# Performance work log

Hardware: AMD Instinct MI355X
Metric: run time of the kernel (lower is better)

Reference implementation:

```python
import jax, jax.numpy as jnp
import numpy as np

V, E, HD, K = 100000, 128, 256, 9
B, T = 128, 512
H = HD // 2  # per-direction hidden size


def setup_inputs() -> dict:
    key = jax.random.key(0)
    ks = jax.random.split(key, 16)
    s = 0.1
    rn = lambda k, shape: jax.random.normal(k, shape, jnp.float32) * s
    sentences = jax.random.randint(ks[0], (B, T), 0, V, dtype=jnp.int32)
    lengths = jax.random.randint(ks[1], (B,), 1, T + 1, dtype=jnp.int32)
    return {
        'sentences': sentences,
        'lengths': lengths,
        'embed': rn(ks[2], (V, E)),
        'Wih_f': rn(ks[3], (4 * H, E)), 'Whh_f': rn(ks[4], (4 * H, H)),
        'bih_f': rn(ks[5], (4 * H,)), 'bhh_f': rn(ks[6], (4 * H,)),
        'Wih_b': rn(ks[7], (4 * H, E)), 'Whh_b': rn(ks[8], (4 * H, H)),
        'bih_b': rn(ks[9], (4 * H,)), 'bhh_b': rn(ks[10], (4 * H,)),
        'W_out': rn(ks[11], (K, HD)), 'b_out': rn(ks[12], (K,)),
        'start_t': rn(ks[13], (K,)), 'end_t': rn(ks[14], (K,)),
        'trans': rn(ks[15], (K, K)),
    }


def _lstm(x, mask, Wih, Whh, bih, bhh, reverse):
    # x: [B,T,E], mask: [B,T] bool. Replicates packed-sequence semantics:
    # state frozen and output zeroed at padding positions (padding is trailing,
    # so reverse=True starts fresh at each sequence's true end).
    Bv, Hv = x.shape[0], Whh.shape[1]
    bias = bih + bhh

    def step(carry, inp):
        h, c = carry
        x_t, m_t = inp  # [B,E], [B,1]
        gates = x_t @ Wih.T + h @ Whh.T + bias  # [B,4H]
        i, f, g, o = jnp.split(gates, 4, axis=-1)  # torch gate order i,f,g,o
        c_new = jax.nn.sigmoid(f) * c + jax.nn.sigmoid(i) * jnp.tanh(g)
        h_new = jax.nn.sigmoid(o) * jnp.tanh(c_new)
        h = jnp.where(m_t, h_new, h)
        c = jnp.where(m_t, c_new, c)
        return (h, c), h * m_t.astype(h.dtype)

    init = (jnp.zeros((Bv, Hv), x.dtype), jnp.zeros((Bv, Hv), x.dtype))
    xs = (jnp.swapaxes(x, 0, 1), jnp.swapaxes(mask, 0, 1)[..., None])
    _, hs = jax.lax.scan(step, init, xs, reverse=reverse)
    return jnp.swapaxes(hs, 0, 1)  # [B,T,H]


def _emissions(sentences, mask, embed, Wih_f, Whh_f, bih_f, bhh_f,
               Wih_b, Whh_b, bih_b, bhh_b, W_out, b_out):
    x = embed[sentences]  # [B,T,E] (dropout is identity at inference)
    hf = _lstm(x, mask, Wih_f, Whh_f, bih_f, bhh_f, reverse=False)
    hb = _lstm(x, mask, Wih_b, Whh_b, bih_b, bhh_b, reverse=True)
    h = jnp.concatenate([hf, hb], axis=-1)  # [B,T,2H]
    return jnp.einsum('btd,kd->btk', h, W_out) + b_out  # [B,T,K]


def _viterbi(em, mask, start_t, end_t, trans):
    # torchcrf-style batched Viterbi decode. em: [B,T,K], mask: [B,T] bool.
    Kv = em.shape[-1]
    ident = jnp.arange(Kv, dtype=jnp.int32)[None]  # identity backpointers for pads
    score0 = start_t[None] + em[:, 0]  # [B,K]

    def step(score, inp):
        em_t, m_t = inp  # [B,K], [B,1]
        cand = score[:, :, None] + trans[None] + em_t[:, None, :]  # [B,K_prev,K_cur]
        new_score = cand.max(axis=1)
        idx = cand.argmax(axis=1).astype(jnp.int32)  # [B,K]
        score = jnp.where(m_t, new_score, score)
        idx = jnp.where(m_t, idx, ident)
        return score, idx

    xs = (jnp.swapaxes(em[:, 1:], 0, 1), jnp.swapaxes(mask[:, 1:], 0, 1)[..., None])
    score, hist = jax.lax.scan(step, score0, xs)  # hist: [T-1,B,K]
    score = score + end_t[None]
    last_tag = jnp.argmax(score, axis=-1).astype(jnp.int32)  # [B]

    def back(tag, idx_t):
        prev = jnp.take_along_axis(idx_t, tag[:, None], axis=1)[:, 0]
        return prev, prev

    _, tags_prev = jax.lax.scan(back, last_tag, hist, reverse=True)  # [T-1,B]
    tags = jnp.swapaxes(jnp.concatenate([tags_prev, last_tag[None]], axis=0), 0, 1)
    return jnp.where(mask, tags, 0), score.max(axis=-1)


def reference(sentences, lengths, embed, Wih_f, Whh_f, bih_f, bhh_f,
              Wih_b, Whh_b, bih_b, bhh_b, W_out, b_out, start_t, end_t, trans):
    mask = jnp.arange(sentences.shape[1])[None] < lengths[:, None]  # [B,T]
    em = _emissions(sentences, mask, embed, Wih_f, Whh_f, bih_f, bhh_f,
                    Wih_b, Whh_b, bih_b, bhh_b, W_out, b_out)
    tags, _ = _viterbi(em, mask, start_t, end_t, trans)
    return tags  # [B,T] int32, padded positions set to 0
```

## Files before the change

### kernel.cpp

```cpp
#include <hip/hip_runtime.h>
#include <cmath>

#define B_  128
#define T_  512
#define E_  128
#define H_  128
#define G4  512
#define K_  9

__global__ __launch_bounds__(256, 2)
void proj_gemm(const int* __restrict__ sent, const float* __restrict__ embed,
               const float* __restrict__ Wf, const float* __restrict__ Wb,
               const float* __restrict__ bif, const float* __restrict__ bhf,
               const float* __restrict__ bib, const float* __restrict__ bhb,
               float* __restrict__ proj, int t0f, int Tc)
{
  __shared__ __align__(16) float Al[128 * 64];
  __shared__ __align__(16) float Bl[128 * 64];
  const int tid   = threadIdx.x;
  const int ntile = blockIdx.x;
  const int mtile = blockIdx.y;
  const int tpb   = Tc >> 6;
  const int b     = mtile / tpb;
  const int toff  = (mtile - b * tpb) << 6;
  const int dir   = ntile >> 3;
  const int t0    = dir ? (T_ - t0f - Tc) : t0f;
  const float* __restrict__ W = dir ? Wb : Wf;
  const int n0 = (ntile & 7) << 6;

  {
    const int r  = tid & 63;
    const int kc = tid >> 6;
    const int t  = t0 + toff + r;
    const int vid = sent[b * T_ + t];
    const float* arow = embed + (size_t)vid * E_ + kc * 32;
    const float* brow = W + (size_t)(n0 + r) * E_ + kc * 32;
#pragma unroll
    for (int q = 0; q < 8; ++q) {
      float4 av = *(const float4*)(arow + q * 4);
      float4 bv = *(const float4*)(brow + q * 4);
      int k0 = kc * 32 + q * 4;
      Al[(k0 + 0) * 64 + r] = av.x; Al[(k0 + 1) * 64 + r] = av.y;
      Al[(k0 + 2) * 64 + r] = av.z; Al[(k0 + 3) * 64 + r] = av.w;
      Bl[(k0 + 0) * 64 + r] = bv.x; Bl[(k0 + 1) * 64 + r] = bv.y;
      Bl[(k0 + 2) * 64 + r] = bv.z; Bl[(k0 + 3) * 64 + r] = bv.w;
    }
  }
  __syncthreads();

  const int mg = tid & 15, ng = tid >> 4;
  float acc[4][4] = {};
#pragma unroll 8
  for (int k = 0; k < 128; ++k) {
    float4 a  = *(const float4*)&Al[k * 64 + mg * 4];
    float4 bb = *(const float4*)&Bl[k * 64 + ng * 4];
    acc[0][0] += a.x * bb.x; acc[0][1] += a.x * bb.y; acc[0][2] += a.x * bb.z; acc[0][3] += a.x * bb.w;
    acc[1][0] += a.y * bb.x; acc[1][1] += a.y * bb.y; acc[1][2] += a.y * bb.z; acc[1][3] += a.y * bb.w;
    acc[2][0] += a.z * bb.x; acc[2][1] += a.z * bb.y; acc[2][2] += a.z * bb.z; acc[2][3] += a.z * bb.w;
    acc[3][0] += a.w * bb.x; acc[3][1] += a.w * bb.y; acc[3][2] += a.w * bb.z; acc[3][3] += a.w * bb.w;
  }

  const float* bi = dir ? bib : bif;
  const float* bh = dir ? bhb : bhf;
  const int nl = ng * 4;
  float4 bias;
  bias.x = bi[n0 + nl + 0] + bh[n0 + nl + 0];
  bias.y = bi[n0 + nl + 1] + bh[n0 + nl + 1];
  bias.z = bi[n0 + nl + 2] + bh[n0 + nl + 2];
  bias.w = bi[n0 + nl + 3] + bh[n0 + nl + 3];
#pragma unroll
  for (int i = 0; i < 4; ++i) {
    const int tloc = toff + mg * 4 + i;
    float4 o;
    o.x = acc[i][0] + bias.x; o.y = acc[i][1] + bias.y;
    o.z = acc[i][2] + bias.z; o.w = acc[i][3] + bias.w;
    *(float4*)&proj[((size_t)(b * Tc + tloc)) * 1024 + dir * G4 + n0 + nl] = o;
  }
}

__global__ __launch_bounds__(512, 2)
void lstm_chunk(const float* __restrict__ proj,
                const float* __restrict__ Whf, const float* __restrict__ Whb,
                const int* __restrict__ lengths,
                float* __restrict__ hs,
                float* __restrict__ sh, float* __restrict__ sc,
                int t0f, int Tc, int first)
{
  const int dir = blockIdx.x;
  const int b   = blockIdx.y;
  const int tid = threadIdx.x;
  const float* __restrict__ Whh = dir ? Whb : Whf;
  __shared__ __align__(16) float h_lds[H_];
  __shared__ float gates[G4];

  float w[128];
  {
    const float* wr = Whh + (size_t)tid * H_;
#pragma unroll
    for (int k = 0; k < 128; k += 4) {
      float4 v = *(const float4*)(wr + k);
      w[k] = v.x; w[k + 1] = v.y; w[k + 2] = v.z; w[k + 3] = v.w;
    }
  }
#pragma unroll
  for (int k = 0; k < 128; ++k) asm volatile("" : "+v"(w[k]));

  const int len = lengths[b];
  const int t0  = dir ? (T_ - t0f - Tc) : t0f;
  float c = 0.f;
  if (tid < H_) {
    if (first) {
      h_lds[tid] = 0.f;
    } else {
      h_lds[tid] = sh[(dir * B_ + b) * H_ + tid];
      c          = sc[(dir * B_ + b) * H_ + tid];
    }
  }
  __syncthreads();

  const float* projp = proj + (size_t)b * Tc * 1024 + dir * G4 + tid;
  float pv = projp[(size_t)(dir ? (Tc - 1) : 0) * 1024];
  for (int s = 0; s < Tc; ++s) {
    const int tc = dir ? (Tc - 1 - s) : s;
    const int t  = t0 + tc;
    float nv = 0.f;
    if (s + 1 < Tc) {
      const int tcn = dir ? (Tc - 2 - s) : (s + 1);
      nv = projp[(size_t)tcn * 1024];
    }
    float a0 = 0.f, a1 = 0.f, a2 = 0.f, a3 = 0.f;
#pragma unroll
    for (int k4 = 0; k4 < 32; ++k4) {
      float4 h4 = *(const float4*)&h_lds[k4 * 4];
      a0 += w[4 * k4 + 0] * h4.x; a1 += w[4 * k4 + 1] * h4.y;
      a2 += w[4 * k4 + 2] * h4.z; a3 += w[4 * k4 + 3] * h4.w;
    }
    float acc = pv + (a0 + a1) + (a2 + a3);
    const int blk = tid >> 7;
    gates[tid] = (blk == 2) ? tanhf(acc) : 1.f / (1.f + expf(-acc));
    __syncthreads();
    if (tid < H_) {
      float gi = gates[tid], gf = gates[tid + 128];
      float gg = gates[tid + 256], go = gates[tid + 384];
      float cn = gf * c + gi * gg;
      float hn = go * tanhf(cn);
      bool  m  = (t < len);
      float hold = h_lds[tid];
      c = m ? cn : c;
      h_lds[tid] = m ? hn : hold;
      hs[(size_t)(b * T_ + t) * 256 + dir * H_ + tid] = m ? hn : 0.f;
    }
    __syncthreads();
    pv = nv;
  }
  if (tid < H_) {
    sh[(dir * B_ + b) * H_ + tid] = h_lds[tid];
    sc[(dir * B_ + b) * H_ + tid] = c;
  }
}

__global__ __launch_bounds__(256)
void emis_kernel(const float* __restrict__ hs, const float* __restrict__ Wout,
                 const float* __restrict__ bout, float* __restrict__ em)
{
  __shared__ __align__(16) float Wl[K_ * 256];
  const int tid = threadIdx.x;
  for (int i = tid; i < K_ * 256; i += 256) Wl[i] = Wout[i];
  __syncthreads();
  const int m = blockIdx.x * 256 + tid;
  const float* h = hs + (size_t)m * 256;
  float acc[K_] = {};
#pragma unroll 4
  for (int kk = 0; kk < 64; ++kk) {
    float4 h4 = *(const float4*)(h + kk * 4);
#pragma unroll
    for (int k9 = 0; k9 < K_; ++k9) {
      float4 w4 = *(const float4*)&Wl[k9 * 256 + kk * 4];
      acc[k9] += h4.x * w4.x + h4.y * w4.y + h4.z * w4.z + h4.w * w4.w;
    }
  }
#pragma unroll
  for (int k9 = 0; k9 < K_; ++k9) em[(size_t)m * K_ + k9] = acc[k9] + bout[k9];
}

__global__ __launch_bounds__(64)
void viterbi_kernel(const float* __restrict__ em, const int* __restrict__ lengths,
                    const float* __restrict__ st, const float* __restrict__ en,
                    const float* __restrict__ trans, int* __restrict__ tags)
{
  const int b    = blockIdx.x;
  const int lane = threadIdx.x;
  __shared__ unsigned char hist[(T_ - 1) * 16];
  const int len = lengths[b];
  float tr[K_];
#pragma unroll
  for (int j = 0; j < K_; ++j) tr[j] = (lane < K_) ? trans[j * K_ + lane] : 0.f;
  float s = (lane < K_) ? st[lane] + em[(size_t)(b * T_) * K_ + lane] : -1e30f;
  for (int t = 1; t < len; ++t) {
    float best = -1e30f; int bj = 0;
#pragma unroll
    for (int j = 0; j < K_; ++j) {
      float v = __shfl(s, j) + tr[j];
      if (v > best) { best = v; bj = j; }
    }
    if (lane < K_) {
      s = best + em[(size_t)(b * T_ + t) * K_ + lane];
      hist[(t - 1) * 16 + lane] = (unsigned char)bj;
    }
  }
  float fs = (lane < K_) ? s + en[lane] : -1e30f;
  float best = -1e30f; int last = 0;
#pragma unroll
  for (int j = 0; j < K_; ++j) {
    float v = __shfl(fs, j);
    if (v > best) { best = v; last = j; }
  }
  __syncthreads();
  if (lane == 0) {
    int tag = last;
    tags[b * T_ + len - 1] = tag;
    for (int t = len - 2; t >= 0; --t) {
      tag = hist[t * 16 + tag];
      tags[b * T_ + t] = tag;
    }
  }
  for (int t = len + lane; t < T_; t += 64) tags[b * T_ + t] = 0;
}

extern "C" void kernel_launch(void* const* d_in, const int* in_sizes, int n_in,
                              void* d_out, int out_size, void* d_ws, size_t ws_size,
                              hipStream_t stream)
{
  const int*   sent  = (const int*)d_in[0];
  const int*   lens  = (const int*)d_in[1];
  const float* embed = (const float*)d_in[2];
  const float* Wif   = (const float*)d_in[3];
  const float* Whf   = (const float*)d_in[4];
  const float* bif   = (const float*)d_in[5];
  const float* bhf   = (const float*)d_in[6];
  const float* Wib   = (const float*)d_in[7];
  const float* Whb   = (const float*)d_in[8];
  const float* bib   = (const float*)d_in[9];
  const float* bhb   = (const float*)d_in[10];
  const float* Wout  = (const float*)d_in[11];
  const float* bout  = (const float*)d_in[12];
  const float* stt   = (const float*)d_in[13];
  const float* ent   = (const float*)d_in[14];
  const float* trans = (const float*)d_in[15];
  int* tags = (int*)d_out;

  float* ws   = (float*)d_ws;
  float* hs   = ws;
  float* em   = hs + (size_t)B_ * T_ * 256;
  float* sh   = em + (size_t)B_ * T_ * K_;
  float* sc   = sh + (size_t)2 * B_ * H_;
  float* proj = sc + (size_t)2 * B_ * H_;
  const size_t fixed_bytes = (size_t)(proj - ws) * sizeof(float);

  int Tc = 512;
  while (Tc > 64 && fixed_bytes + (size_t)B_ * Tc * 1024 * sizeof(float) > ws_size)
    Tc >>= 1;

  const int nch = T_ / Tc;
  for (int c2 = 0; c2 < nch; ++c2) {
    const int t0f = c2 * Tc;
    dim3 g1(16, B_ * (Tc >> 6));
    hipLaunchKernelGGL(proj_gemm, g1, dim3(256), 0, stream,
                       sent, embed, Wif, Wib, bif, bhf, bib, bhb, proj, t0f, Tc);
    dim3 g2(2, B_);
    hipLaunchKernelGGL(lstm_chunk, g2, dim3(512), 0, stream,
                       proj, Whf, Whb, lens, hs, sh, sc, t0f, Tc, (int)(c2 == 0));
  }
  hipLaunchKernelGGL(emis_kernel, dim3((B_ * T_) / 256), dim3(256), 0, stream,
                     hs, Wout, bout, em);
  hipLaunchKernelGGL(viterbi_kernel, dim3(B_), dim3(64), 0, stream,
                     em, lens, stt, ent, trans, tags);
}
```

Measured before the change: 976.4 us.

## Compute LSTM gates in-wave via shuffles with double-buffered hidden state

Recurrent LSTM step is remapped so each lane handles two gate rows over half of the hidden dimension, combining K-halves and gate groups with cross-lane shuffles instead of a shared gates array. All four gates for a hidden unit now land in the same wave, so the cell update is done redundantly per lane and the hidden vector is double-buffered in LDS. This removes one of the two block barriers per timestep along with the LDS gate round trip. The cost is extra shuffles and redundant elementwise work, and the row-to-lane mapping must be exactly right.

New measurement: 940.7 us. 3.6% less time.

```diff
diff --git a/kernel.cpp b/kernel.cpp
--- a/kernel.cpp
+++ b/kernel.cpp
@@ -89,73 +89,94 @@
   const int dir = blockIdx.x;
   const int b   = blockIdx.y;
   const int tid = threadIdx.x;
+  const int l   = tid & 63;
+  const int wv  = tid >> 6;
+  const int u   = wv * 16 + (l & 15);
+  const int gp  = (l >> 4) & 1;
+  const int kh  = l >> 5;
+  const int rowA = u + (gp ? 256 : 0);
+  const int rowB = rowA + 128;
   const float* __restrict__ Whh = dir ? Whb : Whf;
-  __shared__ __align__(16) float h_lds[H_];
-  __shared__ float gates[G4];
-
-  float w[128];
+  __shared__ __align__(16) float h_hist[2][H_];
+
+  float wA[64], wB[64];
   {
-    const float* wr = Whh + (size_t)tid * H_;
-#pragma unroll
-    for (int k = 0; k < 128; k += 4) {
-      float4 v = *(const float4*)(wr + k);
-      w[k] = v.x; w[k + 1] = v.y; w[k + 2] = v.z; w[k + 3] = v.w;
-    }
-  }
-#pragma unroll
-  for (int k = 0; k < 128; ++k) asm volatile("" : "+v"(w[k]));
+    const float* wra = Whh + (size_t)rowA * H_ + kh * 64;
+    const float* wrb = Whh + (size_t)rowB * H_ + kh * 64;
+#pragma unroll
+    for (int k = 0; k < 64; k += 4) {
+      float4 va = *(const float4*)(wra + k);
+      float4 vb = *(const float4*)(wrb + k);
+      wA[k] = va.x; wA[k + 1] = va.y; wA[k + 2] = va.z; wA[k + 3] = va.w;
+      wB[k] = vb.x; wB[k + 1] = vb.y; wB[k + 2] = vb.z; wB[k + 3] = vb.w;
+    }
+  }
+#pragma unroll
+  for (int k = 0; k < 64; ++k) {
+    asm volatile("" : "+v"(wA[k]));
+    asm volatile("" : "+v"(wB[k]));
+  }
 
   const int len = lengths[b];
   const int t0  = dir ? (T_ - t0f - Tc) : t0f;
-  float c = 0.f;
-  if (tid < H_) {
-    if (first) {
-      h_lds[tid] = 0.f;
-    } else {
-      h_lds[tid] = sh[(dir * B_ + b) * H_ + tid];
-      c          = sc[(dir * B_ + b) * H_ + tid];
-    }
-  }
-  __syncthreads();
-
-  const float* projp = proj + (size_t)b * Tc * 1024 + dir * G4 + tid;
-  float pv = projp[(size_t)(dir ? (Tc - 1) : 0) * 1024];
+  float c = 0.f, h_reg = 0.f;
+  if (!first) {
+    c     = sc[(dir * B_ + b) * H_ + u];
+    h_reg = sh[(dir * B_ + b) * H_ + u];
+  }
+  if (l < 16) h_hist[1][u] = h_reg;
+  __syncthreads();
+
+  const float* projpA = proj + (size_t)b * Tc * 1024 + dir * G4 + rowA;
+  const float* projpB = projpA + 128;
+  const int tc00 = dir ? (Tc - 1) : 0;
+  float pvA = projpA[(size_t)tc00 * 1024];
+  float pvB = projpB[(size_t)tc00 * 1024];
+
   for (int s = 0; s < Tc; ++s) {
     const int tc = dir ? (Tc - 1 - s) : s;
     const int t  = t0 + tc;
-    float nv = 0.f;
+    float nvA = 0.f, nvB = 0.f;
     if (s + 1 < Tc) {
       const int tcn = dir ? (Tc - 2 - s) : (s + 1);
-      nv = projp[(size_t)tcn * 1024];
-    }
+      nvA = projpA[(size_t)tcn * 1024];
+      nvB = projpB[(size_t)tcn * 1024];
+    }
+    const float* hp = h_hist[(s + 1) & 1] + kh * 64;
     float a0 = 0.f, a1 = 0.f, a2 = 0.f, a3 = 0.f;
 #pragma unroll
-    for (int k4 = 0; k4 < 32; ++k4) {
-      float4 h4 = *(const float4*)&h_lds[k4 * 4];
-      a0 += w[4 * k4 + 0] * h4.x; a1 += w[4 * k4 + 1] * h4.y;
-      a2 += w[4 * k4 + 2] * h4.z; a3 += w[4 * k4 + 3] * h4.w;
-    }
-    float acc = pv + (a0 + a1) + (a2 + a3);
-    const int blk = tid >> 7;
-    gates[tid] = (blk == 2) ? tanhf(acc) : 1.f / (1.f + expf(-acc));
+    for (int k4 = 0; k4 < 16; ++k4) {
+      float4 h4 = *(const float4*)&hp[k4 * 4];
+      a0 += wA[4 * k4 + 0] * h4.x; a1 += wA[4 * k4 + 1] * h4.y;
+      a0 += wA[4 * k4 + 2] * h4.z; a1 += wA[4 * k4 + 3] * h4.w;
+      a2 += wB[4 * k4 + 0] * h4.x; a3 += wB[4 * k4 + 1] * h4.y;
+      a2 += wB[4 * k4 + 2] * h4.z; a3 += wB[4 * k4 + 3] * h4.w;
+    }
+    float sA = a0 + a1; sA += __shfl_xor(sA, 32); sA += pvA;
+    float sB = a2 + a3; sB += __shfl_xor(sB, 32); sB += pvB;
+    const float gA = gp ? tanhf(sA) : 1.f / (1.f + expf(-sA));
+    const float gB = 1.f / (1.f + expf(-sB));
+    const float xA = __shfl_xor(gA, 16);
+    const float xB = __shfl_xor(gB, 16);
+    const float gi = gp ? xA : gA;
+    const float gf = gp ? xB : gB;
+    const float gg = gp ? gA : xA;
+    const float go = gp ? gB : xB;
+    const float cn = gf * c + gi * gg;
+    const float hn = go * tanhf(cn);
+    const bool  m  = (t < len);
+    c     = m ? cn : c;
+    h_reg = m ? hn : h_reg;
+    if (l < 16) {
+      h_hist[s & 1][u] = h_reg;
+      hs[(size_t)(b * T_ + t) * 256 + dir * H_ + u] = m ? hn : 0.f;
+    }
     __syncthreads();
-    if (tid < H_) {
-      float gi = gates[tid], gf = gates[tid + 128];
-      float gg = gates[tid + 256], go = gates[tid + 384];
-      float cn = gf * c + gi * gg;
-      float hn = go * tanhf(cn);
-      bool  m  = (t < len);
-      float hold = h_lds[tid];
-      c = m ? cn : c;
-      h_lds[tid] = m ? hn : hold;
-      hs[(size_t)(b * T_ + t) * 256 + dir * H_ + tid] = m ? hn : 0.f;
-    }
-    __syncthreads();
-    pv = nv;
-  }
-  if (tid < H_) {
-    sh[(dir * B_ + b) * H_ + tid] = h_lds[tid];
-    sc[(dir * B_ + b) * H_ + tid] = c;
+    pvA = nvA; pvB = nvB;
+  }
+  if (l < 16 && wv == (u >> 4)) {
+    sh[(dir * B_ + b) * H_ + u] = h_reg;
+    sc[(dir * B_ + b) * H_ + u] = c;
   }
 }
 
```
